# Optimization experiments

Hardware: AMD Instinct MI355X
Metric: run time of the kernel (lower is better)

The kernel has to match this reference:

```python
import jax, jax.numpy as jnp
import numpy as np

B, L, D, H = 2, 2048, 1024, 16
HD = D // H  # head_dim = 64


def setup_inputs() -> dict:
    key = jax.random.key(0)
    k1, k2, k3, k4, k5 = jax.random.split(key, 5)
    s = 1.0 / np.sqrt(D)
    return {
        "x": jax.random.normal(k1, (B, L, D), dtype=jnp.float32),
        "quantum_scores": jax.random.normal(k2, (B, L, L), dtype=jnp.float32),
        "wq": jax.random.normal(k3, (D, D), dtype=jnp.float32) * s,
        "wk": jax.random.normal(k4, (D, D), dtype=jnp.float32) * s,
        "wv": jax.random.normal(k5, (D, D), dtype=jnp.float32) * s,
        "scale": jnp.ones((H, 1, 1), dtype=jnp.float32),
    }


def reference(x, quantum_scores, wq, wk, wv, scale):
    Bq, Lq, _ = x.shape
    # nn.Linear: y = x @ W^T ; then split heads -> (B, H, L, HD)
    def split_heads(t):
        return t.reshape(Bq, Lq, H, HD).transpose(0, 2, 1, 3)

    q = split_heads(x @ wq.T)
    k = split_heads(x @ wk.T)
    v = split_heads(x @ wv.T)

    logits = jnp.einsum("bhqd,bhkd->bhqk", q, k) / np.sqrt(HD).astype(np.float32)
    logits = logits + quantum_scores[:, None, :, :]          # quantum bias, broadcast over heads
    logits = logits * scale[None, :, :, :]                   # per-head learnable scale
    attn = jax.nn.softmax(logits, axis=-1)
    out = jnp.einsum("bhqk,bhkd->bhqd", attn, v)
    return out.transpose(0, 2, 1, 3).reshape(Bq, Lq, D)
```

## Files before the change

kernel.cpp:

```cpp
#include <hip/hip_runtime.h>

#define Bq 2
#define Lq 2048
#define Dq 1024
#define Hq 16
#define HDq 64

typedef _Float16 f16;
typedef _Float16 f16x8 __attribute__((ext_vector_type(8)));
typedef _Float16 f16x4 __attribute__((ext_vector_type(4)));
typedef __fp16 hf16x2 __attribute__((ext_vector_type(2)));
typedef float f32x4 __attribute__((ext_vector_type(4)));
typedef float f32x16 __attribute__((ext_vector_type(16)));

__device__ __forceinline__ void gload_lds16(const void* g, void* l) {
    __builtin_amdgcn_global_load_lds(
        (const __attribute__((address_space(1))) unsigned int*)g,
        (__attribute__((address_space(3))) unsigned int*)l, 16, 0, 0);
}

__device__ __forceinline__ void swap32(int& a, int& b) {
    asm volatile("v_permlane32_swap_b32 %0, %1" : "+v"(a), "+v"(b));
}

__device__ __forceinline__ int pk2(float a, float b) {
    hf16x2 v = __builtin_amdgcn_cvt_pkrtz(a, b);
    return __builtin_bit_cast(int, v);
}

__global__ __launch_bounds__(256) void convert_kernel(
    const float* __restrict__ x,
    const float* __restrict__ wq, const float* __restrict__ wk, const float* __restrict__ wv,
    f16* __restrict__ x_h, f16* __restrict__ wq_h, f16* __restrict__ wk_h, f16* __restrict__ wv_h)
{
    const int NX = Bq*Lq*Dq;
    const int NW = Dq*Dq;
    const int total4 = (NX + 3*NW) / 4;
    for (int i = blockIdx.x*blockDim.x + threadIdx.x; i < total4;
         i += gridDim.x*blockDim.x) {
        int e = i * 4;
        const float* src; f16* dst; int off;
        if (e < NX) { src = x; dst = x_h; off = e; }
        else {
            int t = e - NX; int w = t >> 20; off = t & (NW-1);
            src = (w==0) ? wq : (w==1) ? wk : wv;
            dst = (w==0) ? wq_h : (w==1) ? wk_h : wv_h;
        }
        float4 v = *reinterpret_cast<const float4*>(src + off);
        f16x4 hv; hv.x=(f16)v.x; hv.y=(f16)v.y; hv.z=(f16)v.z; hv.w=(f16)v.w;
        *reinterpret_cast<f16x4*>(dst + off) = hv;
    }
}

#define GBM 128
#define GBN 128
#define GBK 32

__global__ __launch_bounds__(256) void qkv_mfma_kernel(
    const f16* __restrict__ x_h,
    const f16* __restrict__ wq_h, const f16* __restrict__ wk_h, const f16* __restrict__ wv_h,
    f16* __restrict__ q_h, f16* __restrict__ k_h, f16* __restrict__ vT_h)
{
    __shared__ __align__(16) f16 As[GBM*GBK];
    __shared__ __align__(16) f16 Bs[GBN*GBK];

    const int tid  = threadIdx.x;
    const int lane = tid & 63;
    const int wave = tid >> 6;
    const int wr = wave >> 1, wc = wave & 1;
    const int l15 = lane & 15, l4 = lane >> 4;
    const int n0 = blockIdx.x * GBN;
    const int m0 = blockIdx.y * GBM;
    const int z  = blockIdx.z;
    const f16* W = (z==0) ? wq_h : (z==1) ? wk_h : wv_h;

    const int sslot = tid & 3;

    f32x4 acc[4][4];
    #pragma unroll
    for (int i=0;i<4;++i)
        #pragma unroll
        for (int j=0;j<4;++j) acc[i][j] = f32x4{0.f,0.f,0.f,0.f};

    for (int kt = 0; kt < Dq; kt += GBK) {
        __syncthreads();
        #pragma unroll
        for (int j = 0; j < 2; ++j) {
            int slotIdx = tid + j*256;
            int row = slotIdx >> 2;
            gload_lds16(x_h + (size_t)(m0+row)*Dq + kt + sslot*8,
                        (char*)As + slotIdx*16);
            gload_lds16(W   + (size_t)(n0+row)*Dq + kt + sslot*8,
                        (char*)Bs + slotIdx*16);
        }
        __syncthreads();

        f16x8 a[4], b[4];
        #pragma unroll
        for (int m=0;m<4;++m) {
            int row = wr*64 + m*16 + l15;
            a[m] = *reinterpret_cast<const f16x8*>((const char*)As + row*64 + l4*16);
        }
        #pragma unroll
        for (int n=0;n<4;++n) {
            int row = wc*64 + n*16 + l15;
            b[n] = *reinterpret_cast<const f16x8*>((const char*)Bs + row*64 + l4*16);
        }
        #pragma unroll
        for (int m=0;m<4;++m)
            #pragma unroll
            for (int n=0;n<4;++n)
                acc[m][n] = __builtin_amdgcn_mfma_f32_16x16x32_f16(a[m], b[n], acc[m][n], 0,0,0);
    }

    #pragma unroll
    for (int m=0;m<4;++m) {
        #pragma unroll
        for (int r=0;r<4;++r) {
            int grow = m0 + wr*64 + m*16 + l4*4 + r;
            int b_   = grow >> 11;
            int lrow = grow & (Lq-1);
            #pragma unroll
            for (int n=0;n<4;++n) {
                int gcol = n0 + wc*64 + n*16 + l15;
                int h = gcol >> 6, d = gcol & 63;
                int bh = b_*Hq + h;
                f16 val = (f16)acc[m][n][r];
                if (z==0)      q_h[((size_t)bh*Lq + lrow)*HDq + d] = val;
                else if (z==1) k_h[((size_t)bh*Lq + lrow)*HDq + d] = val;
                else           vT_h[((size_t)bh*HDq + d)*Lq + lrow] = val;
            }
        }
    }
}

__global__ __launch_bounds__(256) void qm_pre_kernel(
    const float* __restrict__ quantum, f16* __restrict__ qm_pre)
{
    __shared__ float qs[32][64];
    const int tid = threadIdx.x;
    const int qt = blockIdx.x, kt = blockIdx.y, b = blockIdx.z;
    const float* base = quantum + ((size_t)b*Lq + qt*32)*Lq + kt*64;
    #pragma unroll
    for (int i=0;i<2;++i) {
        int idx = tid + i*256;
        int r = idx >> 4, c = (idx & 15)*4;
        float4 v = *reinterpret_cast<const float4*>(base + (size_t)r*Lq + c);
        qs[r][c]=v.x; qs[r][c+1]=v.y; qs[r][c+2]=v.z; qs[r][c+3]=v.w;
    }
    __syncthreads();
    const int seg = tid >> 6, lane = tid & 63, l31 = lane & 31, hi = lane >> 5;
    f16x8 u;
    #pragma unroll
    for (int e=0;e<8;++e) {
        int key = 16*seg + 8*(e>>2) + 4*hi + (e&3);
        u[e] = (f16)qs[l31][key];
    }
    f16* outp = qm_pre + (((size_t)b*32 + kt)*64 + qt)*2048 + seg*512 + lane*8;
    *reinterpret_cast<f16x8*>(outp) = u;
}

__global__ __launch_bounds__(256, 1) void attn64_kernel(
    const f16* __restrict__ q_h, const f16* __restrict__ k_h, const f16* __restrict__ vT_h,
    const f16* __restrict__ qm_pre, const float* __restrict__ scale,
    float* __restrict__ out)
{
    __shared__ __align__(16) char lds[32768];

    const int tid  = threadIdx.x;
    const int lane = tid & 63;
    const int wave = tid >> 6;
    const int l31  = lane & 31;
    const int hi   = lane >> 5;
    const int bh = blockIdx.x;
    const int qb = blockIdx.y;
    const int b_ = bh >> 4, h = bh & 15;
    const int qW = qb*256 + wave*64;
    const int qtA = (qW) >> 5;
    const float sc = scale[h];
    const float c1 = 0.125f * sc * 1.44269504f;
    const float c2 = sc * 1.44269504f;

    const f16* kbase = k_h  + (size_t)bh*Lq*HDq;
    const f16* vbase = vT_h + (size_t)bh*HDq*Lq;

    f16x8 qfA[4], qfB[4];
    {
        const f16* qbA = q_h + ((size_t)bh*Lq + qW + l31)*HDq + hi*8;
        const f16* qbB = qbA + 32*HDq;
        #pragma unroll
        for (int ds=0; ds<4; ++ds) {
            qfA[ds] = *reinterpret_cast<const f16x8*>(qbA + ds*16);
            qfB[ds] = *reinterpret_cast<const f16x8*>(qbB + ds*16);
        }
    }

    f32x16 oA0, oA1, oB0, oB1;
    #pragma unroll
    for (int r=0;r<16;++r) { oA0[r]=0.f; oA1[r]=0.f; oB0[r]=0.f; oB1[r]=0.f; }
    float mA = -1e30f, sA = 0.f, mB = -1e30f, sB = 0.f;

    auto STAGE = [&](int t, int buf) {
        const int k0 = t*64;
        char* LK = lds + buf*16384;
        char* LV = LK + 8192;
        #pragma unroll
        for (int i=0;i<2;++i) {
            int g = tid + i*256;
            int row = g >> 3, slot = g & 7;
            int ss = slot ^ (row & 7);
            gload_lds16(kbase + (size_t)(k0+row)*HDq + ss*8, LK + g*16);
            gload_lds16(vbase + (size_t)row*Lq + k0 + ss*8,  LV + g*16);
        }
    };

    auto HALF = [&](f32x16 st[2], f16x8 qm[4], float& m_run, float& s_run,
                    f32x16& o0, f32x16& o1, f16x8 pb[4]) {
        float lg[32];
        #pragma unroll
        for (int s=0;s<4;++s)
            #pragma unroll
            for (int e=0;e<8;++e) {
                int i = s*8 + e;
                float sv = (i < 16) ? st[0][i] : st[1][i-16];
                lg[i] = sv*c1 + (float)qm[s][e]*c2;
            }
        float tmax = lg[0];
        #pragma unroll
        for (int r=1;r<32;++r) tmax = fmaxf(tmax, lg[r]);
        tmax = fmaxf(tmax, __shfl_xor(tmax, 32));
        if (!__all(tmax <= m_run + 8.f)) {
            float m_new = fmaxf(m_run, tmax);
            float corr = __builtin_amdgcn_exp2f(m_run - m_new);
            m_run = m_new;
            s_run *= corr;
            #pragma unroll
            for (int r=0;r<16;++r) { o0[r] *= corr; o1[r] *= corr; }
        }
        float p[32], ts = 0.f;
        #pragma unroll
        for (int r=0;r<32;++r) { p[r] = __builtin_amdgcn_exp2f(lg[r] - m_run); ts += p[r]; }
        s_run += ts;
        #pragma unroll
        for (int ks=0; ks<4; ++ks) {
            int w0 = pk2(p[8*ks+0], p[8*ks+1]);
            int w1 = pk2(p[8*ks+2], p[8*ks+3]);
            int w2 = pk2(p[8*ks+4], p[8*ks+5]);
            int w3 = pk2(p[8*ks+6], p[8*ks+7]);
            swap32(w0, w2);
            swap32(w1, w3);
            union { int w[4]; f16x8 v; } u;
            u.w[0]=w0; u.w[1]=w1; u.w[2]=w2; u.w[3]=w3;
            pb[ks] = u.v;
        }
    };

    auto COMPUTE = [&](int t, int buf) {
        const char* LK = lds + buf*16384;
        const char* LV = LK + 8192;
        f16x8 qmA[4], qmB[4];
        const f16* qmbA = qm_pre + (((size_t)b_*32 + t)*64 + qtA)*2048 + lane*8;
        #pragma unroll
        for (int s=0;s<4;++s) {
            qmA[s] = *reinterpret_cast<const f16x8*>(qmbA + s*512);
            qmB[s] = *reinterpret_cast<const f16x8*>(qmbA + 2048 + s*512);
        }
        f32x16 stA[2], stB[2];
        #pragma unroll
        for (int kt=0;kt<2;++kt) {
            #pragma unroll
            for (int r=0;r<16;++r) { stA[kt][r]=0.f; stB[kt][r]=0.f; }
            #pragma unroll
            for (int ds=0;ds<4;++ds) {
                f16x8 ka = *reinterpret_cast<const f16x8*>(
                    LK + ((kt*32+l31)<<7) + (((ds*2+hi)^(l31&7))<<4));
                stA[kt] = __builtin_amdgcn_mfma_f32_32x32x16_f16(ka, qfA[ds], stA[kt], 0,0,0);
                stB[kt] = __builtin_amdgcn_mfma_f32_32x32x16_f16(ka, qfB[ds], stB[kt], 0,0,0);
            }
        }
        f16x8 pbA[4], pbB[4];
        HALF(stA, qmA, mA, sA, oA0, oA1, pbA);
        HALF(stB, qmB, mB, sB, oB0, oB1, pbB);
        #pragma unroll
        for (int ks=0; ks<4; ++ks) {
            #pragma unroll
            for (int vt=0; vt<2; ++vt) {
                f16x8 va = *reinterpret_cast<const f16x8*>(
                    LV + ((vt*32+l31)<<7) + (((ks*2+hi)^(l31&7))<<4));
                if (vt==0) {
                    oA0 = __builtin_amdgcn_mfma_f32_32x32x16_f16(va, pbA[ks], oA0, 0,0,0);
                    oB0 = __builtin_amdgcn_mfma_f32_32x32x16_f16(va, pbB[ks], oB0, 0,0,0);
                } else {
                    oA1 = __builtin_amdgcn_mfma_f32_32x32x16_f16(va, pbA[ks], oA1, 0,0,0);
                    oB1 = __builtin_amdgcn_mfma_f32_32x32x16_f16(va, pbB[ks], oB1, 0,0,0);
                }
            }
        }
    };

    STAGE(0, 0);
    STAGE(1, 1);
    for (int t = 0; t < 31; ++t) {
        asm volatile("s_waitcnt vmcnt(4)" ::: "memory");
        __builtin_amdgcn_s_barrier();
        COMPUTE(t, t & 1);
        asm volatile("s_waitcnt lgkmcnt(0)" ::: "memory");
        __builtin_amdgcn_sched_barrier(0);
        __builtin_amdgcn_s_barrier();
        if (t < 30) STAGE(t+2, t & 1);
    }
    asm volatile("s_waitcnt vmcnt(0)" ::: "memory");
    __builtin_amdgcn_s_barrier();
    COMPUTE(31, 1);

    float sAt = sA + __shfl_xor(sA, 32);
    float sBt = sB + __shfl_xor(sB, 32);
    float invA = 1.0f / sAt, invB = 1.0f / sBt;
    float* obA = out + ((size_t)b_*Lq + qW + l31)*Dq + h*HDq;
    float* obB = obA + (size_t)32*Dq;
    #pragma unroll
    for (int r=0;r<16;++r) {
        int drow = (r&3) + 8*(r>>2) + 4*hi;
        obA[drow]      = oA0[r]*invA;
        obA[32 + drow] = oA1[r]*invA;
        obB[drow]      = oB0[r]*invB;
        obB[32 + drow] = oB1[r]*invB;
    }
}

extern "C" void kernel_launch(void* const* d_in, const int* in_sizes, int n_in,
                              void* d_out, int out_size, void* d_ws, size_t ws_size,
                              hipStream_t stream) {
    const float* x       = (const float*)d_in[0];
    const float* quantum = (const float*)d_in[1];
    const float* wq      = (const float*)d_in[2];
    const float* wk      = (const float*)d_in[3];
    const float* wv      = (const float*)d_in[4];
    const float* scale   = (const float*)d_in[5];
    float* out = (float*)d_out;

    f16* ws     = (f16*)d_ws;
    f16* x_h    = ws;
    f16* wq_h   = ws + 4194304;
    f16* wk_h   = ws + 5242880;
    f16* wv_h   = ws + 6291456;
    f16* q_h    = ws + 7340032;
    f16* k_h    = ws + 11534336;
    f16* vT_h   = ws + 15728640;
    f16* qm_pre = ws + 19922944;

    convert_kernel<<<1024, 256, 0, stream>>>(x, wq, wk, wv, x_h, wq_h, wk_h, wv_h);

    dim3 gq(64, 32, 2);
    qm_pre_kernel<<<gq, 256, 0, stream>>>(quantum, qm_pre);

    dim3 g1(Dq/GBN, (Bq*Lq)/GBM, 3);
    qkv_mfma_kernel<<<g1, 256, 0, stream>>>(x_h, wq_h, wk_h, wv_h, q_h, k_h, vT_h);

    dim3 g2(Bq*Hq, Lq/256);
    attn64_kernel<<<g2, 256, 0, stream>>>(q_h, k_h, vT_h, qm_pre, scale, out);
}
```

Baseline: 145.0 us.

## Split attention into 8 waves of 32 queries with two blocks per CU

The attention kernel now runs 512 threads per block, with each of the 8 waves owning 32 query rows instead of 4 waves owning 64. This cuts per-wave register pressure so two blocks can share a CU, and K/V staging is spread across twice as many threads. It also adds s_setprio around the MFMA sections and replaces the serial max and sum reductions with tree reductions. In exchange, each K fragment read from LDS now feeds only one MFMA instead of two, so LDS read traffic per FLOP roughly doubles, and the barriers now synchronise more waves.

```diff
diff --git a/kernel.cpp b/kernel.cpp
--- a/kernel.cpp
+++ b/kernel.cpp
@@ -160,7 +160,7 @@
     *reinterpret_cast<f16x8*>(outp) = u;
 }
 
-__global__ __launch_bounds__(256, 1) void attn64_kernel(
+__global__ __launch_bounds__(512, 2) void attn8_kernel(
     const f16* __restrict__ q_h, const f16* __restrict__ k_h, const f16* __restrict__ vT_h,
     const f16* __restrict__ qm_pre, const float* __restrict__ scale,
     float* __restrict__ out)
@@ -175,8 +175,8 @@
     const int bh = blockIdx.x;
     const int qb = blockIdx.y;
     const int b_ = bh >> 4, h = bh & 15;
-    const int qW = qb*256 + wave*64;
-    const int qtA = (qW) >> 5;
+    const int qW = qb*256 + wave*32;
+    const int qt = qb*8 + wave;
     const float sc = scale[h];
     const float c1 = 0.125f * sc * 1.44269504f;
     const float c2 = sc * 1.44269504f;
@@ -184,38 +184,53 @@
     const f16* kbase = k_h  + (size_t)bh*Lq*HDq;
     const f16* vbase = vT_h + (size_t)bh*HDq*Lq;
 
-    f16x8 qfA[4], qfB[4];
+    f16x8 qf[4];
     {
-        const f16* qbA = q_h + ((size_t)bh*Lq + qW + l31)*HDq + hi*8;
-        const f16* qbB = qbA + 32*HDq;
-        #pragma unroll
-        for (int ds=0; ds<4; ++ds) {
-            qfA[ds] = *reinterpret_cast<const f16x8*>(qbA + ds*16);
-            qfB[ds] = *reinterpret_cast<const f16x8*>(qbB + ds*16);
-        }
-    }
-
-    f32x16 oA0, oA1, oB0, oB1;
-    #pragma unroll
-    for (int r=0;r<16;++r) { oA0[r]=0.f; oA1[r]=0.f; oB0[r]=0.f; oB1[r]=0.f; }
-    float mA = -1e30f, sA = 0.f, mB = -1e30f, sB = 0.f;
+        const f16* qb_ = q_h + ((size_t)bh*Lq + qW + l31)*HDq + hi*8;
+        #pragma unroll
+        for (int ds=0; ds<4; ++ds)
+            qf[ds] = *reinterpret_cast<const f16x8*>(qb_ + ds*16);
+    }
+
+    f32x16 o0, o1;
+    #pragma unroll
+    for (int r=0;r<16;++r) { o0[r]=0.f; o1[r]=0.f; }
+    float m_run = -1e30f, s_run = 0.f;
 
     auto STAGE = [&](int t, int buf) {
         const int k0 = t*64;
         char* LK = lds + buf*16384;
         char* LV = LK + 8192;
-        #pragma unroll
-        for (int i=0;i<2;++i) {
-            int g = tid + i*256;
-            int row = g >> 3, slot = g & 7;
-            int ss = slot ^ (row & 7);
-            gload_lds16(kbase + (size_t)(k0+row)*HDq + ss*8, LK + g*16);
-            gload_lds16(vbase + (size_t)row*Lq + k0 + ss*8,  LV + g*16);
-        }
+        int row = tid >> 3, slot = tid & 7;
+        int ss = slot ^ (row & 7);
+        gload_lds16(kbase + (size_t)(k0+row)*HDq + ss*8, LK + tid*16);
+        gload_lds16(vbase + (size_t)row*Lq + k0 + ss*8,  LV + tid*16);
     };
 
-    auto HALF = [&](f32x16 st[2], f16x8 qm[4], float& m_run, float& s_run,
-                    f32x16& o0, f32x16& o1, f16x8 pb[4]) {
+    auto COMPUTE = [&](int t, int buf) {
+        const char* LK = lds + buf*16384;
+        const char* LV = LK + 8192;
+        f16x8 qm[4];
+        const f16* qmb = qm_pre + (((size_t)b_*32 + t)*64 + qt)*2048 + lane*8;
+        #pragma unroll
+        for (int s=0;s<4;++s)
+            qm[s] = *reinterpret_cast<const f16x8*>(qmb + s*512);
+
+        f32x16 st[2];
+        __builtin_amdgcn_s_setprio(1);
+        #pragma unroll
+        for (int kt=0;kt<2;++kt) {
+            #pragma unroll
+            for (int r=0;r<16;++r) st[kt][r]=0.f;
+            #pragma unroll
+            for (int ds=0;ds<4;++ds) {
+                f16x8 ka = *reinterpret_cast<const f16x8*>(
+                    LK + ((kt*32+l31)<<7) + (((ds*2+hi)^(l31&7))<<4));
+                st[kt] = __builtin_amdgcn_mfma_f32_32x32x16_f16(ka, qf[ds], st[kt], 0,0,0);
+            }
+        }
+        __builtin_amdgcn_s_setprio(0);
+
         float lg[32];
         #pragma unroll
         for (int s=0;s<4;++s)
@@ -225,10 +240,16 @@
                 float sv = (i < 16) ? st[0][i] : st[1][i-16];
                 lg[i] = sv*c1 + (float)qm[s][e]*c2;
             }
-        float tmax = lg[0];
-        #pragma unroll
-        for (int r=1;r<32;++r) tmax = fmaxf(tmax, lg[r]);
-        tmax = fmaxf(tmax, __shfl_xor(tmax, 32));
+
+        float tm[16];
+        #pragma unroll
+        for (int r=0;r<16;++r) tm[r] = fmaxf(lg[r], lg[r+16]);
+        #pragma unroll
+        for (int w=8; w>0; w>>=1)
+            #pragma unroll
+            for (int r=0;r<w;++r) tm[r] = fmaxf(tm[r], tm[r+w]);
+        float tmax = fmaxf(tm[0], __shfl_xor(tm[0], 32));
+
         if (!__all(tmax <= m_run + 8.f)) {
             float m_new = fmaxf(m_run, tmax);
             float corr = __builtin_amdgcn_exp2f(m_run - m_new);
@@ -237,10 +258,20 @@
             #pragma unroll
             for (int r=0;r<16;++r) { o0[r] *= corr; o1[r] *= corr; }
         }
-        float p[32], ts = 0.f;
-        #pragma unroll
-        for (int r=0;r<32;++r) { p[r] = __builtin_amdgcn_exp2f(lg[r] - m_run); ts += p[r]; }
-        s_run += ts;
+
+        float p[32];
+        #pragma unroll
+        for (int r=0;r<32;++r) p[r] = __builtin_amdgcn_exp2f(lg[r] - m_run);
+        float sm[16];
+        #pragma unroll
+        for (int r=0;r<16;++r) sm[r] = p[r] + p[r+16];
+        #pragma unroll
+        for (int w=8; w>0; w>>=1)
+            #pragma unroll
+            for (int r=0;r<w;++r) sm[r] += sm[r+w];
+        s_run += sm[0];
+
+        f16x8 pb[4];
         #pragma unroll
         for (int ks=0; ks<4; ++ks) {
             int w0 = pk2(p[8*ks+0], p[8*ks+1]);
@@ -253,55 +284,24 @@
             u.w[0]=w0; u.w[1]=w1; u.w[2]=w2; u.w[3]=w3;
             pb[ks] = u.v;
         }
-    };
-
-    auto COMPUTE = [&](int t, int buf) {
-        const char* LK = lds + buf*16384;
-        const char* LV = LK + 8192;
-        f16x8 qmA[4], qmB[4];
-        const f16* qmbA = qm_pre + (((size_t)b_*32 + t)*64 + qtA)*2048 + lane*8;
-        #pragma unroll
-        for (int s=0;s<4;++s) {
-            qmA[s] = *reinterpret_cast<const f16x8*>(qmbA + s*512);
-            qmB[s] = *reinterpret_cast<const f16x8*>(qmbA + 2048 + s*512);
-        }
-        f32x16 stA[2], stB[2];
-        #pragma unroll
-        for (int kt=0;kt<2;++kt) {
-            #pragma unroll
-            for (int r=0;r<16;++r) { stA[kt][r]=0.f; stB[kt][r]=0.f; }
-            #pragma unroll
-            for (int ds=0;ds<4;++ds) {
-                f16x8 ka = *reinterpret_cast<const f16x8*>(
-                    LK + ((kt*32+l31)<<7) + (((ds*2+hi)^(l31&7))<<4));
-                stA[kt] = __builtin_amdgcn_mfma_f32_32x32x16_f16(ka, qfA[ds], stA[kt], 0,0,0);
-                stB[kt] = __builtin_amdgcn_mfma_f32_32x32x16_f16(ka, qfB[ds], stB[kt], 0,0,0);
-            }
-        }
-        f16x8 pbA[4], pbB[4];
-        HALF(stA, qmA, mA, sA, oA0, oA1, pbA);
-        HALF(stB, qmB, mB, sB, oB0, oB1, pbB);
+
+        __builtin_amdgcn_s_setprio(1);
         #pragma unroll
         for (int ks=0; ks<4; ++ks) {
-            #pragma unroll
-            for (int vt=0; vt<2; ++vt) {
-                f16x8 va = *reinterpret_cast<const f16x8*>(
-                    LV + ((vt*32+l31)<<7) + (((ks*2+hi)^(l31&7))<<4));
-                if (vt==0) {
-                    oA0 = __builtin_amdgcn_mfma_f32_32x32x16_f16(va, pbA[ks], oA0, 0,0,0);
-                    oB0 = __builtin_amdgcn_mfma_f32_32x32x16_f16(va, pbB[ks], oB0, 0,0,0);
-                } else {
-                    oA1 = __builtin_amdgcn_mfma_f32_32x32x16_f16(va, pbA[ks], oA1, 0,0,0);
-                    oB1 = __builtin_amdgcn_mfma_f32_32x32x16_f16(va, pbB[ks], oB1, 0,0,0);
-                }
-            }
-        }
+            f16x8 va0 = *reinterpret_cast<const f16x8*>(
+                LV + (l31<<7)        + (((ks*2+hi)^(l31&7))<<4));
+            f16x8 va1 = *reinterpret_cast<const f16x8*>(
+                LV + ((32+l31)<<7)   + (((ks*2+hi)^(l31&7))<<4));
+            o0 = __builtin_amdgcn_mfma_f32_32x32x16_f16(va0, pb[ks], o0, 0,0,0);
+            o1 = __builtin_amdgcn_mfma_f32_32x32x16_f16(va1, pb[ks], o1, 0,0,0);
+        }
+        __builtin_amdgcn_s_setprio(0);
     };
 
     STAGE(0, 0);
     STAGE(1, 1);
     for (int t = 0; t < 31; ++t) {
-        asm volatile("s_waitcnt vmcnt(4)" ::: "memory");
+        asm volatile("s_waitcnt vmcnt(2)" ::: "memory");
         __builtin_amdgcn_s_barrier();
         COMPUTE(t, t & 1);
         asm volatile("s_waitcnt lgkmcnt(0)" ::: "memory");
@@ -313,18 +313,14 @@
     __builtin_amdgcn_s_barrier();
     COMPUTE(31, 1);
 
-    float sAt = sA + __shfl_xor(sA, 32);
-    float sBt = sB + __shfl_xor(sB, 32);
-    float invA = 1.0f / sAt, invB = 1.0f / sBt;
-    float* obA = out + ((size_t)b_*Lq + qW + l31)*Dq + h*HDq;
-    float* obB = obA + (size_t)32*Dq;
+    float s_tot = s_run + __shfl_xor(s_run, 32);
+    float inv = 1.0f / s_tot;
+    float* ob = out + ((size_t)b_*Lq + qW + l31)*Dq + h*HDq;
     #pragma unroll
     for (int r=0;r<16;++r) {
         int drow = (r&3) + 8*(r>>2) + 4*hi;
-        obA[drow]      = oA0[r]*invA;
-        obA[32 + drow] = oA1[r]*invA;
-        obB[drow]      = oB0[r]*invB;
-        obB[32 + drow] = oB1[r]*invB;
+        ob[drow]      = o0[r]*inv;
+        ob[32 + drow] = o1[r]*inv;
     }
 }
 
@@ -358,5 +354,5 @@
     qkv_mfma_kernel<<<g1, 256, 0, stream>>>(x_h, wq_h, wk_h, wv_h, q_h, k_h, vT_h);
 
     dim3 g2(Bq*Hq, Lq/256);
-    attn64_kernel<<<g2, 256, 0, stream>>>(q_h, k_h, vT_h, qm_pre, scale, out);
-}
+    attn8_kernel<<<g2, 512, 0, stream>>>(q_h, k_h, vT_h, qm_pre, scale, out);
+}
```

After: 137.7 us. -5.0%, faster.
